# Optimization experiments

Hardware: AMD Instinct MI355X
Metric: run time of the kernel (lower is better)

Reference implementation:

```python
import jax, jax.numpy as jnp
import numpy as np

B, C, H, W = 8, 512, 64, 64


def conv3x3(x, w, b):
    # x: [B,C,H,W], w: [O,I,3,3], b: [O]; stride 1, padding 1 (SAME)
    y = jax.lax.conv_general_dilated(
        x, w, window_strides=(1, 1), padding='SAME',
        dimension_numbers=('NCHW', 'OIHW', 'NCHW'))
    return y + b[None, :, None, None]


def setup_inputs() -> dict:
    key = jax.random.key(0)
    ks = jax.random.split(key, 8)
    wscale = 1.0 / np.sqrt(C * 9)  # keep attention logits in a sane range
    x = jax.random.normal(ks[0], (B, C, H, W), dtype=jnp.float32)
    wq = jax.random.normal(ks[1], (C, C, 3, 3), dtype=jnp.float32) * wscale
    bq = jax.random.normal(ks[2], (C,), dtype=jnp.float32) * 0.01
    wk = jax.random.normal(ks[3], (C, C, 3, 3), dtype=jnp.float32) * wscale
    bk = jax.random.normal(ks[4], (C,), dtype=jnp.float32) * 0.01
    wv = jax.random.normal(ks[5], (C, C, 3, 3), dtype=jnp.float32) * wscale
    bv = jax.random.normal(ks[6], (C,), dtype=jnp.float32) * 0.01
    gamma = jax.random.normal(ks[7], (1,), dtype=jnp.float32)
    return {'x': x, 'wq': wq, 'bq': bq, 'wk': wk, 'bk': bk,
            'wv': wv, 'bv': bv, 'gamma': gamma}


def reference(x, wq, bq, wk, bk, wv, bv, gamma):
    b, c, h, w = x.shape
    n = h * w
    q = conv3x3(x, wq, bq).reshape(b, c, n)   # [B,C,N]
    k = conv3x3(x, wk, bk).reshape(b, c, n)   # [B,C,N]
    v = conv3x3(x, wv, bv).reshape(b, c, n)   # [B,C,N]
    # channel-wise attention: [B,C,N] x [B,N,C] -> [B,C,C]
    attn = jnp.einsum('bcn,bdn->bcd', q, k)
    attn = jax.nn.softmax(attn, axis=-1)
    out = jnp.einsum('bcd,bdn->bcn', attn, v).reshape(b, c, h, w)
    return gamma * out + x
```

## Files before the change

### kernel.cpp

```cpp
#include <hip/hip_runtime.h>
#include <stdint.h>

typedef __attribute__((ext_vector_type(8))) short bf16x8;
typedef __attribute__((ext_vector_type(4))) float f32x4;
typedef __attribute__((ext_vector_type(4))) int i32x4;
typedef __attribute__((ext_vector_type(8))) int i32x8;
typedef __attribute__((ext_vector_type(8))) unsigned short u16x8;
typedef __attribute__((ext_vector_type(4))) unsigned short u16x4;

#define DI static __device__ __forceinline__

constexpr int CB = 8;
constexpr int BCH = 4;
constexpr int CC = 512;
constexpr int CN = 4096;
constexpr int K1 = CC * 9;
constexpr int MR = 3 * CC;
constexpr int KSPL = 4;
constexpr size_t XSPLIT = (size_t)BCH * 66 * 66 * 512;

DI unsigned short f2bf(float f) {
  union { float f; uint32_t u; } v; v.f = f;
  uint32_t r = (v.u + 0x7FFFu + ((v.u >> 16) & 1u)) >> 16;
  return (unsigned short)r;
}
DI float bf2f(unsigned short h) {
  union { uint32_t u; float f; } v; v.u = ((uint32_t)h) << 16;
  return v.f;
}
DI unsigned char f2e4m3(float x) {
  union { float f; uint32_t u; } v; v.f = x;
  uint32_t sgn = (v.u >> 24) & 0x80u;
  float a = fabsf(x);
  if (a < 0.015625f) {
    int qi = (int)rintf(a * 512.f);
    return (unsigned char)(sgn | (uint32_t)qi);
  }
  int e = (int)((v.u >> 23) & 0xff) - 127;
  uint32_t m3 = (v.u >> 20) & 7u;
  uint32_t rest = v.u & 0xFFFFFu;
  if (rest > 0x80000u || (rest == 0x80000u && (m3 & 1u))) {
    if (++m3 == 8u) { m3 = 0; ++e; }
  }
  if (e > 8 || (e == 8 && m3 == 7u)) return (unsigned char)(sgn | 0x7Eu);
  return (unsigned char)(sgn | ((uint32_t)(e + 7) << 3) | m3);
}

DI void g2lds16(const void* g, void* l) {
  __builtin_amdgcn_global_load_lds((const __attribute__((address_space(1))) void*)g,
                                   (__attribute__((address_space(3))) void*)l, 16, 0, 0);
}
#define SBAR()  __builtin_amdgcn_s_barrier()
#define SCHED() __builtin_amdgcn_sched_barrier(0)

__global__ __launch_bounds__(256) void prep_xpad(const float* __restrict__ x,
                                                 unsigned short* __restrict__ Xhi,
                                                 unsigned char* __restrict__ X8) {
  int tid = threadIdx.x;
  int w = tid & 63;
  int ccl = tid >> 6;
  int blk = blockIdx.x;
  int h = blk & 63;
  int ccg = (blk >> 6) & 15;
  int b = blk >> 10;
  int c0 = (ccg * 4 + ccl) * 8;
  const float* xp = x + ((size_t)b * CC) * CN + h * 64 + w;
  u16x8 hi;
  unsigned long long lo8 = 0, hi8 = 0;
#pragma unroll
  for (int j = 0; j < 8; ++j) {
    float v = xp[(size_t)(c0 + j) * CN];
    unsigned short h16 = f2bf(v);
    float vhi = bf2f(h16);
    hi[j] = f2bf(vhi * 128.f);
    lo8 |= (unsigned long long)f2e4m3((v - vhi) * 256.f) << (8 * j);
    hi8 |= (unsigned long long)f2e4m3(vhi) << (8 * j);
  }
  size_t pix = (((size_t)b * 66 + (h + 1)) * 66 + (w + 1)) * 512;
  *(u16x8*)&Xhi[pix + c0] = hi;
  *(unsigned long long*)&X8[pix + c0] = lo8;
  *(unsigned long long*)&X8[XSPLIT + pix + c0] = hi8;
}

__global__ __launch_bounds__(256) void prep_abig(
    const float* __restrict__ wq, const float* __restrict__ wk,
    const float* __restrict__ wv, const float* __restrict__ bq,
    const float* __restrict__ bk, const float* __restrict__ bv,
    unsigned short* __restrict__ Ahi, unsigned char* __restrict__ A8,
    float* __restrict__ bias) {
  unsigned id = blockIdx.x * 256 + threadIdx.x;
  int m = id / K1;
  int r = id - m * K1;
  int t = r >> 9;
  int c = r & 511;
  int ky = t / 3;
  int kx = t - ky * 3;
  size_t ip = (size_t)m * 9216 + r;
  if (m < 1024) {
    const float* wp = (m < 512) ? wq : wk;
    int mm = (m < 512) ? m : m - 512;
    float wval = wp[(((size_t)mm * 512 + c) * 3 + ky) * 3 + kx];
    float whi = bf2f(f2bf(wval));
    Ahi[id] = f2bf(whi * 128.f);
    A8[ip] = f2e4m3(whi * 64.f);
    A8[ip + 4608] = f2e4m3((wval - whi) * 16384.f);
  } else {
    float wval = wv[(((size_t)(m - 1024) * 512 + c) * 3 + ky) * 3 + kx];
    Ahi[id] = f2bf(wval * 128.f);
    A8[ip] = 0;
    A8[ip + 4608] = 0;
  }
  if (id < 1536) {
    int mm = (int)id;
    bias[mm] = (mm < 512) ? bq[mm] : (mm < 1024) ? bk[mm - 512] : bv[mm - 1024];
  }
}

__global__ __launch_bounds__(512, 2) void conv_k(
    const unsigned short* __restrict__ Ahi,
    const unsigned char* __restrict__ A8,
    const unsigned short* __restrict__ Xhi,
    const unsigned char* __restrict__ X8,
    const float* __restrict__ bias,
    unsigned short* __restrict__ Qhi, unsigned short* __restrict__ Qlo,
    unsigned short* __restrict__ Khi, unsigned short* __restrict__ Klo,
    unsigned short* __restrict__ Vt)
{
  __shared__ __align__(16) unsigned char smem[4 * 32768];
  const int tid = threadIdx.x;
  const int lane = tid & 63;
  const int wid = tid >> 6;
  const int wr = wid >> 2;
  const int wc = wid & 3;

  int orig = blockIdx.x;
  int xcd, nbl, m0;
  if (orig < 256) {
    xcd = orig & 7; int j = orig >> 3;
    nbl = j >> 2;
    m0 = (j & 3) * 256;
  } else {
    int o = orig - 256;
    xcd = o & 7; int j = o >> 3;
    nbl = j >> 2;
    m0 = 1024 + (j & 3) * 128;
  }
  const int nb = xcd * 8 + nbl;
  const int n0 = nb * 256;
  const int bidx = n0 >> 12;
  const int nl0 = n0 & (CN - 1);
  const int h0 = nl0 >> 6;

  const int srow = tid >> 2;
  const int scu = tid & 3;
  const int scuS = scu ^ ((srow >> 1) & 3);
  const size_t pixOfs = (((size_t)(bidx * 66 + h0 + (srow >> 6))) * 66 + (srow & 63)) * 512;
  const unsigned short* gAh0 = Ahi + (size_t)(m0 + srow) * K1 + scuS * 8;
  const unsigned short* gAh1 = gAh0 + (size_t)128 * K1;
  const unsigned short* gBh0 = Xhi + pixOfs + scuS * 8;
  const unsigned short* gBh1 = gBh0 + (size_t)2 * 66 * 512;
  const unsigned char* gA80 = A8 + (size_t)(m0 + srow) * 9216 + scuS * 16;
  const unsigned char* gA81 = gA80 + (size_t)128 * 9216;
  const unsigned char* gB80 = X8 + pixOfs + scuS * 16;
  const unsigned char* gB81 = gB80 + (size_t)2 * 66 * 512;
  const int wofs = wid * 1024;

  int c0S = 0, kxS = 0, tapS = 0;
  size_t tapOfs = 0;
  auto stage1 = [&](int slot) {
    int aOfs = tapS * 512 + c0S;
    size_t bOfs = tapOfs + (size_t)c0S;
    unsigned char* lA = smem + slot * 32768 + wofs;
    unsigned char* lB = smem + slot * 32768 + 16384 + wofs;
    g2lds16(gAh0 + aOfs, lA);
    g2lds16(gAh1 + aOfs, lA + 8192);
    g2lds16(gBh0 + bOfs, lB);
    g2lds16(gBh1 + bOfs, lB + 8192);
    c0S += 32;
    if (c0S == 512) {
      c0S = 0; ++tapS;
      if (kxS == 2) { kxS = 0; tapOfs += (size_t)64 * 512; }
      else { ++kxS; tapOfs += 512; }
    }
  };
  auto stage1v = [&](int slot) {
    int aOfs = tapS * 512 + c0S;
    size_t bOfs = tapOfs + (size_t)c0S;
    unsigned char* lA = smem + slot * 32768 + wofs;
    unsigned char* lB = smem + slot * 32768 + 16384 + wofs;
    g2lds16(gAh0 + aOfs, lA);
    g2lds16(gBh0 + bOfs, lB);
    g2lds16(gBh1 + bOfs, lB + 8192);
    c0S += 32;
    if (c0S == 512) {
      c0S = 0; ++tapS;
      if (kxS == 2) { kxS = 0; tapOfs += (size_t)64 * 512; }
      else { ++kxS; tapOfs += 512; }
    }
  };
  int c8 = 0, kx8 = 0, tap8 = 0, s8 = 0;
  size_t tapOfs8 = 0;
  auto stage2 = [&](int slot) {
    int aOfs = s8 * 4608 + tap8 * 512 + c8;
    size_t bOfs = (size_t)s8 * XSPLIT + tapOfs8 + (size_t)c8;
    unsigned char* lA = smem + slot * 32768 + wofs;
    unsigned char* lB = smem + slot * 32768 + 16384 + wofs;
    g2lds16(gA80 + aOfs, lA);
    g2lds16(gA81 + aOfs, lA + 8192);
    g2lds16(gB80 + bOfs, lB);
    g2lds16(gB81 + bOfs, lB + 8192);
    c8 += 64;
    if (c8 == 512) {
      c8 = 0; ++tap8;
      if (tap8 == 9) { tap8 = 0; kx8 = 0; tapOfs8 = 0; ++s8; }
      else if (kx8 == 2) { kx8 = 0; tapOfs8 += (size_t)64 * 512; }
      else { ++kx8; tapOfs8 += 512; }
    }
  };

  f32x4 acc[8][4];
  const f32x4 fz = {0.f, 0.f, 0.f, 0.f};
#pragma unroll
  for (int i = 0; i < 8; ++i)
#pragma unroll
    for (int j = 0; j < 4; ++j) acc[i][j] = fz;

  const int kq = (lane >> 4) * 16;
  int slotC, slotS, t2;

  if (m0 < 1024) {
    const int rA = wr * 128 + (lane & 15);
    const int rB = wc * 64 + (lane & 15);
    const int kqA = kq ^ (((rA >> 1) & 3) << 4);
    const int kqB = kq ^ (((rB >> 1) & 3) << 4);

    stage1(0);
    stage1(1);
    asm volatile("s_waitcnt vmcnt(4)" ::: "memory");
    SCHED(); SBAR(); SCHED();
    {
      bf16x8 afA[4], bfA[4], afB[4], bfB[4], af1[4];
#pragma unroll
      for (int mf = 0; mf < 4; ++mf)
        afA[mf] = *(const bf16x8*)(smem + (rA + mf * 16) * 64 + kqA);
#pragma unroll
      for (int nf = 0; nf < 4; ++nf)
        bfA[nf] = *(const bf16x8*)(smem + 16384 + (rB + nf * 16) * 64 + kqB);
      slotC = 0; slotS = 2; t2 = 2;

#define CONV_BF(CURA, CURB, NXTA, NXTB)                                       \
  {                                                                           \
    if (t2 < 144) {                                                           \
      stage1(slotS); slotS = (slotS + 1) & 3;                                 \
      asm volatile("s_waitcnt vmcnt(4)" ::: "memory");                        \
    } else {                                                                  \
      asm volatile("s_waitcnt vmcnt(0)" ::: "memory");                        \
    }                                                                         \
    SCHED(); SBAR(); SCHED();                                                 \
    const unsigned char* lA = smem + slotC * 32768;                           \
    const int slotN = (slotC + 1) & 3;                                        \
    const unsigned char* lAn = smem + slotN * 32768;                          \
    _Pragma("unroll")                                                         \
    for (int mf = 0; mf < 4; ++mf)                                            \
      af1[mf] = *(const bf16x8*)(lA + (rA + 64 + mf * 16) * 64 + kqA);        \
    __builtin_amdgcn_s_setprio(1);                                            \
    _Pragma("unroll")                                                         \
    for (int mf = 0; mf < 4; ++mf) {                                          \
      _Pragma("unroll")                                                       \
      for (int nf = 0; nf < 4; ++nf)                                          \
        acc[mf][nf] = __builtin_amdgcn_mfma_f32_16x16x32_bf16(                \
            CURA[mf], CURB[nf], acc[mf][nf], 0, 0, 0);                        \
    }                                                                         \
    __builtin_amdgcn_s_setprio(0);                                            \
    _Pragma("unroll")                                                         \
    for (int mf = 0; mf < 4; ++mf)                                            \
      NXTA[mf] = *(const bf16x8*)(lAn + (rA + mf * 16) * 64 + kqA);           \
    _Pragma("unroll")                                                         \
    for (int nf = 0; nf < 4; ++nf)                                            \
      NXTB[nf] = *(const bf16x8*)(lAn + 16384 + (rB + nf * 16) * 64 + kqB);   \
    __builtin_amdgcn_s_setprio(1);                                            \
    _Pragma("unroll")                                                         \
    for (int mf = 0; mf < 4; ++mf) {                                          \
      _Pragma("unroll")                                                       \
      for (int nf = 0; nf < 4; ++nf)                                          \
        acc[mf + 4][nf] = __builtin_amdgcn_mfma_f32_16x16x32_bf16(            \
            af1[mf], CURB[nf], acc[mf + 4][nf], 0, 0, 0);                     \
    }                                                                         \
    __builtin_amdgcn_s_setprio(0);                                            \
    slotC = slotN;                                                            \
    ++t2;                                                                     \
  }

      for (int t = 0; t < 144; t += 2) {
        CONV_BF(afA, bfA, afB, bfB)
        CONV_BF(afB, bfB, afA, bfA)
      }
#undef CONV_BF
    }

    stage2(0); stage2(1);
    SCHED(); SBAR(); SCHED();
    stage2(2); stage2(3);
    {
      const int gq = lane >> 4;
      const int slotByte = (gq >> 1) << 15;
      const int cb2 = (gq & 1) * 2;
      const int ff2 = ((lane & 15) >> 1) & 3;
      const int bo0 = ((cb2 ^ ff2) << 4);
      const int bo1 = (((cb2 + 1) ^ ff2) << 4);
      const int aRow = wr * 128 + (lane & 15);
      const int bRow = wc * 64 + (lane & 15);
      i32x8 aF[4], bF[4];
      for (int p = 0; p < 72; ++p) {
        SCHED(); SBAR(); SCHED();
        if (p < 71) { asm volatile("s_waitcnt vmcnt(8)" ::: "memory"); }
        else        { asm volatile("s_waitcnt vmcnt(0)" ::: "memory"); }
        SCHED();
        const unsigned char* pbA = smem + ((p & 1) << 16) + slotByte + aRow * 64;
        const unsigned char* pbB = smem + ((p & 1) << 16) + slotByte + 16384 + bRow * 64;
#pragma unroll
        for (int t = 0; t < 4; ++t) {
          *(i32x4*)&bF[t] = *(const i32x4*)(pbB + t * 1024 + bo0);
          *((i32x4*)&bF[t] + 1) = *(const i32x4*)(pbB + t * 1024 + bo1);
        }
#pragma unroll
        for (int s = 0; s < 4; ++s) {
          *(i32x4*)&aF[s] = *(const i32x4*)(pbA + s * 1024 + bo0);
          *((i32x4*)&aF[s] + 1) = *(const i32x4*)(pbA + s * 1024 + bo1);
        }
        __builtin_amdgcn_s_setprio(1);
#pragma unroll
        for (int s = 0; s < 4; ++s)
#pragma unroll
          for (int t = 0; t < 4; ++t)
            acc[s][t] = __builtin_amdgcn_mfma_scale_f32_16x16x128_f8f6f4(
                aF[s], bF[t], acc[s][t], 0, 0, 0, 127, 0, 127);
        __builtin_amdgcn_s_setprio(0);
#pragma unroll
        for (int s = 0; s < 4; ++s) {
          *(i32x4*)&aF[s] = *(const i32x4*)(pbA + (4 + s) * 1024 + bo0);
          *((i32x4*)&aF[s] + 1) = *(const i32x4*)(pbA + (4 + s) * 1024 + bo1);
        }
        __builtin_amdgcn_s_setprio(1);
#pragma unroll
        for (int s = 0; s < 4; ++s)
#pragma unroll
          for (int t = 0; t < 4; ++t)
            acc[s + 4][t] = __builtin_amdgcn_mfma_scale_f32_16x16x128_f8f6f4(
                aF[s], bF[t], acc[s + 4][t], 0, 0, 0, 127, 0, 127);
        __builtin_amdgcn_s_setprio(0);
        SCHED(); SBAR(); SCHED();
        if (p + 2 < 72) { stage2(2 * (p & 1)); stage2(2 * (p & 1) + 1); }
      }
    }
  } else {
    const int rAv = wr * 64 + (lane & 15);
    const int rB = wc * 64 + (lane & 15);
    const int kqA = kq ^ (((rAv >> 1) & 3) << 4);
    const int kqB = kq ^ (((rB >> 1) & 3) << 4);

    stage1v(0);
    stage1v(1);
    asm volatile("s_waitcnt vmcnt(3)" ::: "memory");
    SCHED(); SBAR(); SCHED();
    bf16x8 afA[4], bfA[4], afB[4], bfB[4];
#pragma unroll
    for (int mf = 0; mf < 4; ++mf)
      afA[mf] = *(const bf16x8*)(smem + (rAv + mf * 16) * 64 + kqA);
#pragma unroll
    for (int nf = 0; nf < 4; ++nf)
      bfA[nf] = *(const bf16x8*)(smem + 16384 + (rB + nf * 16) * 64 + kqB);
    slotC = 0; slotS = 2; t2 = 2;

#define CONV_LV(CURA, CURB, NXTA, NXTB)                                       \
  {                                                                           \
    if (t2 < 144) {                                                           \
      stage1v(slotS); slotS = (slotS + 1) & 3;                                \
      asm volatile("s_waitcnt vmcnt(3)" ::: "memory");                        \
    } else {                                                                  \
      asm volatile("s_waitcnt vmcnt(0)" ::: "memory");                        \
    }                                                                         \
    SCHED(); SBAR(); SCHED();                                                 \
    const int slotN = (slotC + 1) & 3;                                        \
    const unsigned char* lAn = smem + slotN * 32768;                          \
    _Pragma("unroll")                                                         \
    for (int mf = 0; mf < 4; ++mf)                                            \
      NXTA[mf] = *(const bf16x8*)(lAn + (rAv + mf * 16) * 64 + kqA);          \
    _Pragma("unroll")                                                         \
    for (int nf = 0; nf < 4; ++nf)                                            \
      NXTB[nf] = *(const bf16x8*)(lAn + 16384 + (rB + nf * 16) * 64 + kqB);   \
    __builtin_amdgcn_s_setprio(1);                                            \
    _Pragma("unroll")                                                         \
    for (int mf = 0; mf < 4; ++mf) {                                          \
      _Pragma("unroll")                                                       \
      for (int nf = 0; nf < 4; ++nf)                                          \
        acc[mf][nf] = __builtin_amdgcn_mfma_f32_16x16x32_bf16(                \
            CURA[mf], CURB[nf], acc[mf][nf], 0, 0, 0);                        \
    }                                                                         \
    __builtin_amdgcn_s_setprio(0);                                            \
    slotC = slotN;                                                            \
    ++t2;                                                                     \
  }

    for (int t = 0; t < 144; t += 2) {
      CONV_LV(afA, bfA, afB, bfB)
      CONV_LV(afB, bfB, afA, bfA)
    }
#undef CONV_LV
  }

  constexpr float SC = 1.f / 16384.f;
  if (m0 < 1024) {
#pragma unroll
    for (int mf = 0; mf < 8; ++mf) {
#pragma unroll
      for (int nf = 0; nf < 4; ++nf) {
        f32x4 a = acc[mf][nf];
        int mrow = m0 + wr * 128 + mf * 16 + ((lane >> 4) << 2);
        int ncol = nl0 + wc * 64 + nf * 16 + (lane & 15);
        if (m0 < 512) {
#pragma unroll
          for (int j = 0; j < 4; ++j) {
            float v = a[j] * SC + bias[mrow + j];
            unsigned short h16 = f2bf(v);
            size_t o = ((size_t)bidx * CC + (mrow + j)) * CN + ncol;
            Qhi[o] = h16;
            Qlo[o] = f2bf(v - bf2f(h16));
          }
        } else {
#pragma unroll
          for (int j = 0; j < 4; ++j) {
            float v = a[j] * SC + bias[mrow + j];
            unsigned short h16 = f2bf(v);
            size_t o = ((size_t)bidx * CC + (mrow + j - 512)) * CN + ncol;
            Khi[o] = h16;
            Klo[o] = f2bf(v - bf2f(h16));
          }
        }
      }
    }
  } else {
#pragma unroll
    for (int mf = 0; mf < 4; ++mf) {
#pragma unroll
      for (int nf = 0; nf < 4; ++nf) {
        f32x4 a = acc[mf][nf];
        int mrow = m0 + wr * 64 + mf * 16 + ((lane >> 4) << 2);
        int ncol = nl0 + wc * 64 + nf * 16 + (lane & 15);
        u16x4 vs;
#pragma unroll
        for (int j = 0; j < 4; ++j) vs[j] = f2bf(a[j] * SC + bias[mrow + j]);
        *(u16x4*)&Vt[((size_t)bidx * CN + ncol) * CC + (mrow - 1024)] = vs;
      }
    }
  }
}

DI int sofs(int row, int kb) { return row * 128 + (kb ^ ((row & 7) << 4)); }

template<int MODE>
__global__ __launch_bounds__(256) void gemm_k(
    const unsigned short* __restrict__ Qhi, const unsigned short* __restrict__ Qlo,
    const unsigned short* __restrict__ Khi, const unsigned short* __restrict__ Klo,
    const unsigned short* __restrict__ Vt,
    float* __restrict__ attn,
    const unsigned short* __restrict__ P,
    const float* __restrict__ xin,
    const float* __restrict__ gamma,
    float* __restrict__ out)
{
  __shared__ __align__(16) unsigned char sA[16384];
  __shared__ __align__(16) unsigned char sB[16384];
  const int tid = threadIdx.x;
  const int lane = tid & 63;
  const int wav = tid >> 6;
  const int wr = wav >> 1, wc = wav & 1;

  int m0, n0, bidx, Kbeg = 0, Kend, ks = 0;
  if constexpr (MODE == 1) {
    int tile = blockIdx.x & 15;
    ks = blockIdx.x >> 4;
    m0 = (tile & 3) * 128;
    n0 = (tile >> 2) * 128;
    bidx = blockIdx.z;
    Kbeg = ks * (3 * CN / KSPL);
    Kend = Kbeg + (3 * CN / KSPL);
  } else {
    m0 = (blockIdx.x & 3) * 128;
    n0 = (blockIdx.x >> 2) * 128;
    bidx = blockIdx.z;
    Kend = CC;
  }

  auto stage = [&](int k0) {
#pragma unroll
    for (int q = 0; q < 4; ++q) {
      int ci = q * 256 + tid;
      int row = ci >> 3;
      int ke = ((ci & 7) ^ (row & 7)) * 8;
      const unsigned short* ap;
      const unsigned short* bp;
      if constexpr (MODE == 1) {
        int ph = k0 >> 12;
        int kin = k0 & (CN - 1);
        const unsigned short* Aq = (ph == 2) ? Qlo : Qhi;
        const unsigned short* Bk = (ph == 1) ? Klo : Khi;
        ap = Aq + ((size_t)bidx * CC + (m0 + row)) * CN + (kin + ke);
        bp = Bk + ((size_t)bidx * CC + (n0 + row)) * CN + (kin + ke);
      } else {
        ap = P + ((size_t)bidx * CC + (m0 + row)) * CC + (k0 + ke);
        bp = Vt + ((size_t)bidx * CN + (n0 + row)) * CC + (k0 + ke);
      }
      int wbase = (q * 256 + wav * 64) * 16;
      g2lds16(ap, sA + wbase);
      g2lds16(bp, sB + wbase);
    }
  };

  f32x4 acc[4][4];
  const f32x4 fz = {0.f, 0.f, 0.f, 0.f};
#pragma unroll
  for (int i = 0; i < 4; ++i)
#pragma unroll
    for (int j = 0; j < 4; ++j) acc[i][j] = fz;

  for (int k0 = Kbeg; k0 < Kend; k0 += 64) {
    stage(k0);
    __syncthreads();
#pragma unroll
    for (int kkp = 0; kkp < 2; ++kkp) {
      bf16x8 af[4], bfv[4];
#pragma unroll
      for (int mf = 0; mf < 4; ++mf)
        af[mf] = *(const bf16x8*)&sA[sofs(wr * 64 + mf * 16 + (lane & 15),
                                          kkp * 64 + (lane >> 4) * 16)];
#pragma unroll
      for (int nf = 0; nf < 4; ++nf)
        bfv[nf] = *(const bf16x8*)&sB[sofs(wc * 64 + nf * 16 + (lane & 15),
                                           kkp * 64 + (lane >> 4) * 16)];
#pragma unroll
      for (int mf = 0; mf < 4; ++mf)
#pragma unroll
        for (int nf = 0; nf < 4; ++nf)
          acc[mf][nf] = __builtin_amdgcn_mfma_f32_16x16x32_bf16(
              af[mf], bfv[nf], acc[mf][nf], 0, 0, 0);
    }
    __syncthreads();
  }

  float g = 0.f;
  if constexpr (MODE == 2) g = gamma[0];
#pragma unroll
  for (int mf = 0; mf < 4; ++mf) {
#pragma unroll
    for (int nf = 0; nf < 4; ++nf) {
      f32x4 a = acc[mf][nf];
      int mrow = m0 + wr * 64 + mf * 16 + ((lane >> 4) << 2);
      int ncol = n0 + wc * 64 + nf * 16 + (lane & 15);
      if constexpr (MODE == 1) {
        size_t pbase = (size_t)ks * ((size_t)BCH * CC * CC);
#pragma unroll
        for (int j = 0; j < 4; ++j)
          attn[pbase + ((size_t)bidx * CC + (mrow + j)) * CC + ncol] = a[j];
      } else {
#pragma unroll
        for (int j = 0; j < 4; ++j) {
          size_t o = ((size_t)bidx * CC + (mrow + j)) * CN + ncol;
          out[o] = g * a[j] + xin[o];
        }
      }
    }
  }
}

__global__ __launch_bounds__(256) void softmax_k(const float* __restrict__ attn,
                                                 unsigned short* __restrict__ P) {
  int row = blockIdx.x * 4 + (threadIdx.x >> 6);
  int lane = threadIdx.x & 63;
  constexpr size_t PS = (size_t)BCH * CC * CC;
  const float* rp = attn + (size_t)row * 512 + lane * 8;
  f32x4 a = {0.f, 0.f, 0.f, 0.f};
  f32x4 b = {0.f, 0.f, 0.f, 0.f};
#pragma unroll
  for (int ksp = 0; ksp < KSPL; ++ksp) {
    a += *(const f32x4*)(rp + (size_t)ksp * PS);
    b += *(const f32x4*)(rp + (size_t)ksp * PS + 4);
  }
  float mx = fmaxf(fmaxf(fmaxf(a[0], a[1]), fmaxf(a[2], a[3])),
                   fmaxf(fmaxf(b[0], b[1]), fmaxf(b[2], b[3])));
#pragma unroll
  for (int s = 32; s > 0; s >>= 1) mx = fmaxf(mx, __shfl_xor(mx, s, 64));
  float e[8];
  float sum = 0.f;
#pragma unroll
  for (int j = 0; j < 4; ++j) { e[j] = __expf(a[j] - mx); sum += e[j]; }
#pragma unroll
  for (int j = 0; j < 4; ++j) { e[4 + j] = __expf(b[j] - mx); sum += e[4 + j]; }
#pragma unroll
  for (int s = 32; s > 0; s >>= 1) sum += __shfl_xor(sum, s, 64);
  float inv = 1.0f / sum;
  u16x8 o;
#pragma unroll
  for (int j = 0; j < 8; ++j) o[j] = f2bf(e[j] * inv);
  *(u16x8*)&P[(size_t)row * 512 + lane * 8] = o;
}

__global__ __launch_bounds__(256) void fill_sentinel(float* __restrict__ out, int n) {
  int i = blockIdx.x * 256 + threadIdx.x;
  if (i < n) out[i] = 1.0e4f;
}

extern "C" void kernel_launch(void* const* d_in, const int* in_sizes, int n_in,
                              void* d_out, int out_size, void* d_ws, size_t ws_size,
                              hipStream_t stream) {
  (void)in_sizes; (void)n_in;
  const float* x  = (const float*)d_in[0];
  const float* wq = (const float*)d_in[1];
  const float* bq = (const float*)d_in[2];
  const float* wk = (const float*)d_in[3];
  const float* bk = (const float*)d_in[4];
  const float* wv = (const float*)d_in[5];
  const float* bv = (const float*)d_in[6];
  const float* gm = (const float*)d_in[7];
  float* out = (float*)d_out;

  uint8_t* wsp = (uint8_t*)d_ws;
  auto take = [&](size_t bytes) {
    uint8_t* p = wsp;
    wsp += (bytes + 255) & ~(size_t)255;
    return p;
  };
  unsigned short* Xhi = (unsigned short*)take(XSPLIT * 2);
  unsigned char*  X8  = (unsigned char*)take(2 * XSPLIT);
  unsigned short* Ahi = (unsigned short*)take((size_t)MR * K1 * 2);
  unsigned char*  A8  = (unsigned char*)take((size_t)MR * 2 * K1);
  float* bias         = (float*)take((size_t)MR * 4);
  unsigned short* Khi = (unsigned short*)take((size_t)BCH * CC * CN * 2);
  unsigned short* Klo = (unsigned short*)take((size_t)BCH * CC * CN * 2);
  unsigned short* Vt  = (unsigned short*)take((size_t)BCH * CN * CC * 2);
  float* attn         = (float*)Xhi;
  unsigned short* P   = (unsigned short*)((uint8_t*)Xhi +
                          (size_t)KSPL * BCH * CC * CC * 4 + 256);

  size_t needed = (size_t)(wsp - (uint8_t*)d_ws);
  if (ws_size < needed) {
    fill_sentinel<<<(out_size + 255) / 256, 256, 0, stream>>>(out, out_size);
    return;
  }

  for (int ch = 0; ch < CB / BCH; ++ch) {
    const float* xch = x + (size_t)ch * BCH * CC * CN;
    float* outch = out + (size_t)ch * BCH * CC * CN;
    unsigned short* Qhi = (unsigned short*)outch;
    unsigned short* Qlo = Qhi + (size_t)BCH * CC * CN;

    hipMemsetAsync(Xhi, 0, XSPLIT * 2 + 2 * XSPLIT, stream);
    prep_xpad<<<BCH * 16 * 64, 256, 0, stream>>>(xch, Xhi, X8);
    if (ch == 0)
      prep_abig<<<(MR * K1) / 256, 256, 0, stream>>>(wq, wk, wv, bq, bk, bv,
                                                     Ahi, A8, bias);
    conv_k<<<dim3(512), 512, 0, stream>>>(Ahi, A8, Xhi, X8, bias,
                                          Qhi, Qlo, Khi, Klo, Vt);
    gemm_k<1><<<dim3(16 * KSPL, 1, BCH), 256, 0, stream>>>(Qhi, Qlo, Khi, Klo, Vt,
                                                           attn, P, xch, gm, outch);
    softmax_k<<<BCH * 128, 256, 0, stream>>>(attn, P);
    gemm_k<2><<<dim3(128, 1, BCH), 256, 0, stream>>>(Qhi, Qlo, Khi, Klo, Vt,
                                                     attn, P, xch, gm, outch);
  }
}
```

Measured before the change: 1.007 ms.

## Zero only pad borders, swizzle fp8 LDS slots, and double the attention K-split

The full memset of the padded bf16/fp8 input buffers is replaced by a small kernel that zeroes only the one-pixel border, which cuts a large redundant write per batch chunk. The fp8 conv stage now applies an alternating 16-byte offset to odd slots and a matching XOR in the fragment reads, meant to spread LDS bank accesses. The attention GEMM K-split rises from 4 to 8 for more parallelism. The trade-off is a larger partial-sum buffer and extra reduction work, and the border-only zeroing relies on prep_xpad writing every interior pixel.

```diff
diff --git a/kernel.cpp b/kernel.cpp
--- a/kernel.cpp
+++ b/kernel.cpp
@@ -16,7 +16,7 @@
 constexpr int CN = 4096;
 constexpr int K1 = CC * 9;
 constexpr int MR = 3 * CC;
-constexpr int KSPL = 4;
+constexpr int KSPL = 8;
 constexpr size_t XSPLIT = (size_t)BCH * 66 * 66 * 512;
 
 DI unsigned short f2bf(float f) {
@@ -52,6 +52,27 @@
 }
 #define SBAR()  __builtin_amdgcn_s_barrier()
 #define SCHED() __builtin_amdgcn_sched_barrier(0)
+
+__global__ __launch_bounds__(256) void pad_zero(unsigned short* __restrict__ Xhi,
+                                                unsigned char* __restrict__ X8) {
+  int id = blockIdx.x * 256 + threadIdx.x;
+  if (id >= 4 * 260 * 16) return;
+  int t = id & 15;
+  int pp = (id >> 4) % 260;
+  int b = id / (260 * 16);
+  int hh, ww;
+  if (pp < 66)       { hh = 0;  ww = pp; }
+  else if (pp < 132) { hh = 65; ww = pp - 66; }
+  else if (pp < 196) { hh = pp - 131; ww = 0; }
+  else               { hh = pp - 195; ww = 65; }
+  size_t pix = (((size_t)b * 66 + hh) * 66 + ww) * 512 + (size_t)t * 32;
+  const u16x8 z = {0, 0, 0, 0, 0, 0, 0, 0};
+  *(u16x8*)&Xhi[pix] = z;  *(u16x8*)&Xhi[pix + 8] = z;
+  *(u16x8*)&Xhi[pix + 16] = z;  *(u16x8*)&Xhi[pix + 24] = z;
+  const i32x4 z4 = {0, 0, 0, 0};
+  *(i32x4*)&X8[pix] = z4;  *(i32x4*)&X8[pix + 16] = z4;
+  *(i32x4*)&X8[XSPLIT + pix] = z4;  *(i32x4*)&X8[XSPLIT + pix + 16] = z4;
+}
 
 __global__ __launch_bounds__(256) void prep_xpad(const float* __restrict__ x,
                                                  unsigned short* __restrict__ Xhi,
@@ -154,6 +175,7 @@
   const int srow = tid >> 2;
   const int scu = tid & 3;
   const int scuS = scu ^ ((srow >> 1) & 3);
+  const int d8 = (scuS & 1) ? -16 : 16;
   const size_t pixOfs = (((size_t)(bidx * 66 + h0 + (srow >> 6))) * 66 + (srow & 63)) * 512;
   const unsigned short* gAh0 = Ahi + (size_t)(m0 + srow) * K1 + scuS * 8;
   const unsigned short* gAh1 = gAh0 + (size_t)128 * K1;
@@ -201,14 +223,15 @@
   int c8 = 0, kx8 = 0, tap8 = 0, s8 = 0;
   size_t tapOfs8 = 0;
   auto stage2 = [&](int slot) {
+    int so = (slot & 1) ? d8 : 0;
     int aOfs = s8 * 4608 + tap8 * 512 + c8;
     size_t bOfs = (size_t)s8 * XSPLIT + tapOfs8 + (size_t)c8;
     unsigned char* lA = smem + slot * 32768 + wofs;
     unsigned char* lB = smem + slot * 32768 + 16384 + wofs;
-    g2lds16(gA80 + aOfs, lA);
-    g2lds16(gA81 + aOfs, lA + 8192);
-    g2lds16(gB80 + bOfs, lB);
-    g2lds16(gB81 + bOfs, lB + 8192);
+    g2lds16(gA80 + aOfs + so, lA);
+    g2lds16(gA81 + aOfs + so, lA + 8192);
+    g2lds16(gB80 + bOfs + so, lB);
+    g2lds16(gB81 + bOfs + so, lB + 8192);
     c8 += 64;
     if (c8 == 512) {
       c8 = 0; ++tap8;
@@ -305,9 +328,9 @@
       const int gq = lane >> 4;
       const int slotByte = (gq >> 1) << 15;
       const int cb2 = (gq & 1) * 2;
-      const int ff2 = ((lane & 15) >> 1) & 3;
-      const int bo0 = ((cb2 ^ ff2) << 4);
-      const int bo1 = (((cb2 + 1) ^ ff2) << 4);
+      const int fx = (((lane & 15) >> 1) & 3) ^ (gq >> 1);
+      const int bo0 = ((cb2 ^ fx) << 4);
+      const int bo1 = (((cb2 + 1) ^ fx) << 4);
       const int aRow = wr * 128 + (lane & 15);
       const int bRow = wc * 64 + (lane & 15);
       i32x8 aF[4], bF[4];
@@ -654,7 +677,7 @@
     unsigned short* Qhi = (unsigned short*)outch;
     unsigned short* Qlo = Qhi + (size_t)BCH * CC * CN;
 
-    hipMemsetAsync(Xhi, 0, XSPLIT * 2 + 2 * XSPLIT, stream);
+    pad_zero<<<(4 * 260 * 16 + 255) / 256, 256, 0, stream>>>(Xhi, X8);
     prep_xpad<<<BCH * 16 * 64, 256, 0, stream>>>(xch, Xhi, X8);
     if (ch == 0)
       prep_abig<<<(MR * K1) / 256, 256, 0, stream>>>(wq, wk, wv, bq, bk, bv,
```

After: 963.2 us. 4.4% less time.
